# Optimization experiments

Hardware: AMD Instinct MI355X
Metric: run time of the kernel (lower is better)

## Reference

```python
import jax, jax.numpy as jnp
import numpy as np

N = 100_000   # nodes
E = 800_000   # directed edges
D = 300       # emb_dim
L = 5         # num GIN layers
G = 4096      # graphs in batch
FEAT = 512
PROJ = 256
EPS = 1e-5


def setup_inputs() -> dict:
    key = jax.random.key(0)
    ks = jax.random.split(key, 20)
    s = 0.05
    return {
        "atom_type": jax.random.randint(ks[0], (N,), 0, 119, dtype=jnp.int32),
        "chirality": jax.random.randint(ks[1], (N,), 0, 3, dtype=jnp.int32),
        "edge_index": jax.random.randint(ks[2], (2, E), 0, N, dtype=jnp.int32),
        "bond_type": jax.random.randint(ks[3], (E,), 0, 4, dtype=jnp.int32),
        "bond_dir": jax.random.randint(ks[4], (E,), 0, 3, dtype=jnp.int32),
        "batch": jnp.sort(jax.random.randint(ks[5], (N,), 0, G, dtype=jnp.int32)),
        "x_emb1": jax.random.normal(ks[6], (119, D), jnp.float32) * s,
        "x_emb2": jax.random.normal(ks[7], (3, D), jnp.float32) * s,
        "ee1": jax.random.normal(ks[8], (L, 5, D), jnp.float32) * s,
        "ee2": jax.random.normal(ks[9], (L, 3, D), jnp.float32) * s,
        "W1": jax.random.normal(ks[10], (L, D, 2 * D), jnp.float32) * s,
        "b1": jnp.zeros((L, 2 * D), jnp.float32),
        "W2": jax.random.normal(ks[11], (L, 2 * D, D), jnp.float32) * s,
        "b2": jnp.zeros((L, D), jnp.float32),
        "gamma": jnp.ones((L, D), jnp.float32),
        "beta": jnp.zeros((L, D), jnp.float32),
        "feat_W": jax.random.normal(ks[12], (D, FEAT), jnp.float32) * s,
        "feat_b": jnp.zeros((FEAT,), jnp.float32),
        "proj_W": jax.random.normal(ks[13], (FEAT, PROJ), jnp.float32) * s,
        "proj_b": jnp.zeros((PROJ,), jnp.float32),
    }


def _encoder(atom_type, chirality, edge_index, bond_type, bond_dir, batch,
             x_emb1, x_emb2, ee1, ee2, W1, b1, W2, b2, gamma, beta,
             feat_W, feat_b, proj_W, proj_b):
    # Initial node embedding: x_embedding1(x[:,0]) + x_embedding2(x[:,1])
    h = x_emb1[atom_type] + x_emb2[chirality]            # [N, D]
    row, col = edge_index[0], edge_index[1]
    for l in range(L):
        # edge embeddings for real edges
        ee = ee1[l][bond_type] + ee2[l][bond_dir]        # [E, D]
        # gather + add + scatter-sum over real edges
        msgs = h[col] + ee                               # [E, D]
        agg = jax.ops.segment_sum(msgs, row, num_segments=N)  # [N, D]
        # self-loop edges have attr [4, 0] -> constant embedding per layer
        agg = agg + h + (ee1[l, 4] + ee2[l, 0])
        # 2-layer MLP
        hid = jax.nn.relu(agg @ W1[l] + b1[l])
        h2 = hid @ W2[l] + b2[l]
        # BatchNorm1d (training mode: batch statistics, biased variance)
        mean = jnp.mean(h2, axis=0)
        var = jnp.var(h2, axis=0)
        h = gamma[l] * (h2 - mean) * jax.lax.rsqrt(var + EPS) + beta[l]
        if l < L - 1:
            h = jax.nn.relu(h)
    # global mean pool per graph
    sums = jax.ops.segment_sum(h, batch, num_segments=G)              # [G, D]
    counts = jax.ops.segment_sum(jnp.ones((N, 1), h.dtype), batch, num_segments=G)
    pooled = sums / jnp.maximum(counts, 1.0)
    feat = pooled @ feat_W + feat_b                                    # [G, FEAT]
    return feat @ proj_W + proj_b                                      # [G, PROJ]


def reference(atom_type, chirality, edge_index, bond_type, bond_dir, batch,
              x_emb1, x_emb2, ee1, ee2, W1, b1, W2, b2, gamma, beta,
              feat_W, feat_b, proj_W, proj_b):
    return _encoder(atom_type, chirality, edge_index, bond_type, bond_dir, batch,
                    x_emb1, x_emb2, ee1, ee2, W1, b1, W2, b2, gamma, beta,
                    feat_W, feat_b, proj_W, proj_b)
```

## Files before the change

kernel.cpp:

```cpp
#include <hip/hip_runtime.h>
#include <hip/hip_bf16.h>

typedef __bf16 bf16_t;
typedef bf16_t bf16x8 __attribute__((ext_vector_type(8)));
typedef float f32x4 __attribute__((ext_vector_type(4)));

#define D_DIM 300
#define HSTRIDE 304
#define CSTRIDE 304
#define ROWU 152
#define AROWU 160
#define TPB 320

__device__ inline f32x4 mfma16(bf16x8 a, bf16x8 b, f32x4 c) {
  return __builtin_amdgcn_mfma_f32_16x16x32_bf16(a, b, c, 0, 0, 0);
}

__device__ inline void split2(float x, unsigned short& h, unsigned short& l) {
  bf16_t hb = (bf16_t)x;
  float hf = (float)hb;
  bf16_t lb = (bf16_t)(x - hf);
  h = __builtin_bit_cast(unsigned short, hb);
  l = __builtin_bit_cast(unsigned short, lb);
}

__device__ inline uint4 pack8(const unsigned short* s) {
  return make_uint4((unsigned int)s[0] | ((unsigned int)s[1] << 16),
                    (unsigned int)s[2] | ((unsigned int)s[3] << 16),
                    (unsigned int)s[4] | ((unsigned int)s[5] << 16),
                    (unsigned int)s[6] | ((unsigned int)s[7] << 16));
}

__device__ inline unsigned int packbf2(float x0, float x1) {
  unsigned short a = __builtin_bit_cast(unsigned short, (bf16_t)x0);
  unsigned short b = __builtin_bit_cast(unsigned short, (bf16_t)x1);
  return (unsigned int)a | ((unsigned int)b << 16);
}

__device__ inline float bfu_lo(unsigned int u) {
  unsigned int x = u << 16;
  float f;
  __builtin_memcpy(&f, &x, 4);
  return f;
}

__device__ inline float bfu_hi(unsigned int u) {
  unsigned int x = u & 0xffff0000u;
  float f;
  __builtin_memcpy(&f, &x, 4);
  return f;
}


__global__ void zero_u32_kernel(unsigned int* __restrict__ p, long long n) {
  long long i = (long long)blockIdx.x * blockDim.x + threadIdx.x;
  long long s = (long long)gridDim.x * blockDim.x;
  for (; i < n; i += s) p[i] = 0u;
}


__global__ void init_h_kernel(const int* __restrict__ atom, const int* __restrict__ chir,
                              const float* __restrict__ e1, const float* __restrict__ e2,
                              unsigned int* __restrict__ hb) {
  int n = blockIdx.x;
  int t = threadIdx.x;
  if (t >= ROWU) return;
  int d = t * 2;
  unsigned int out = 0u;
  if (d < D_DIM) {
    int a = atom[n], c = chir[n];
    float x0 = e1[a * D_DIM + d] + e2[c * D_DIM + d];
    float x1 = e1[a * D_DIM + d + 1] + e2[c * D_DIM + d + 1];
    out = packbf2(x0, x1);
  }
  hb[(size_t)n * ROWU + t] = out;
}

__global__ void combo_kernel(const float* __restrict__ ee1, const float* __restrict__ ee2,
                             float* __restrict__ ct) {
  int l = blockIdx.x / 13, c = blockIdx.x % 13;
  int d = threadIdx.x;
  if (d >= CSTRIDE) return;
  int bt = (c < 12) ? (c / 3) : 4;
  int bd = (c < 12) ? (c % 3) : 0;
  float v = 0.f;
  if (d < D_DIM)
    v = ee1[(size_t)(l * 5 + bt) * D_DIM + d] + ee2[(size_t)(l * 3 + bd) * D_DIM + d];
  ct[((size_t)(l * 13 + c)) * CSTRIDE + d] = v;
}

__global__ void edge_combo_kernel(const int* __restrict__ bt, const int* __restrict__ bd,
                                  int* __restrict__ ec, int E) {
  int e = blockIdx.x * blockDim.x + threadIdx.x;
  if (e < E) ec[e] = bt[e] * 3 + bd[e];
}


__global__ void csr_count_kernel(const int* __restrict__ row, int* __restrict__ deg, int E) {
  int e = blockIdx.x * blockDim.x + threadIdx.x;
  if (e < E) atomicAdd(&deg[row[e]], 1);
}

#define SBLK 1024
__global__ void scan1_kernel(const int* __restrict__ deg, int* __restrict__ off,
                             int* __restrict__ btot, int n) {
  __shared__ int buf[SBLK];
  int t = threadIdx.x;
  int i = blockIdx.x * SBLK + t;
  int v = (i < n) ? deg[i] : 0;
  buf[t] = v;
  __syncthreads();
#pragma unroll
  for (int s = 1; s < SBLK; s <<= 1) {
    int add = (t >= s) ? buf[t - s] : 0;
    __syncthreads();
    buf[t] += add;
    __syncthreads();
  }
  if (i < n) off[i] = buf[t] - v;
  if (t == SBLK - 1) btot[blockIdx.x] = buf[t];
}

__global__ void scan2_kernel(int* __restrict__ btot, int* __restrict__ off, int n, int nb) {
  __shared__ int buf[128];
  int t = threadIdx.x;
  int v = (t < nb) ? btot[t] : 0;
  buf[t] = v;
  __syncthreads();
#pragma unroll
  for (int s = 1; s < 128; s <<= 1) {
    int add = (t >= s) ? buf[t - s] : 0;
    __syncthreads();
    buf[t] += add;
    __syncthreads();
  }
  if (t < nb) btot[t] = buf[t] - v;
  if (t == nb - 1) off[n] = buf[t];
}

__global__ void scan3_kernel(int* __restrict__ off, int* __restrict__ cur,
                             const int* __restrict__ btot, int n) {
  int i = blockIdx.x * SBLK + threadIdx.x;
  if (i < n) {
    int v = off[i] + btot[blockIdx.x];
    off[i] = v;
    cur[i] = v;
  }
}

__global__ void csr_fill_kernel(const int* __restrict__ row, const int* __restrict__ col,
                                const int* __restrict__ ec, int* __restrict__ cur,
                                unsigned int* __restrict__ pck, int E) {
  int e = blockIdx.x * blockDim.x + threadIdx.x;
  if (e < E) {
    int r = row[e];
    int p = atomicAdd(&cur[r], 1);
    pck[p] = ((unsigned int)col[e] << 4) | (unsigned int)ec[e];
  }
}


__global__ void goff_kernel(const int* __restrict__ batch, int* __restrict__ goff, int N, int G) {
  int n = blockIdx.x * blockDim.x + threadIdx.x;
  if (n >= N) return;
  if (n == 0) {
    int g1 = batch[0];
    for (int g = 0; g <= g1; ++g) goff[g] = 0;
  } else {
    int g0 = batch[n - 1], g1 = batch[n];
    for (int g = g0 + 1; g <= g1; ++g) goff[g] = n;
  }
  if (n == N - 1) {
    int g0 = batch[N - 1];
    for (int g = g0 + 1; g <= G; ++g) goff[g] = N;
  }
}


__global__ void affine_kernel(const float* __restrict__ h2, const float* __restrict__ sc,
                              const float* __restrict__ sh, unsigned int* __restrict__ hb,
                              long long total) {
  long long i = (long long)blockIdx.x * blockDim.x + threadIdx.x;
  long long s = (long long)gridDim.x * blockDim.x;
  for (; i < total; i += s) {
    int cu = (int)(i % ROWU);
    long long n = i / ROWU;
    int d = cu * 2;
    unsigned int out = 0u;
    if (d < D_DIM) {
      float2 v = *(const float2*)(h2 + n * HSTRIDE + d);
      float x0 = fmaxf(fmaf(v.x, sc[d], sh[d]), 0.f);
      float x1 = fmaxf(fmaf(v.y, sc[d + 1], sh[d + 1]), 0.f);
      out = packbf2(x0, x1);
    }
    hb[i] = out;
  }
}


__global__ __launch_bounds__(256) void gather_kernel(
    const unsigned int* __restrict__ hb, const int* __restrict__ off,
    const unsigned int* __restrict__ pck, const float* __restrict__ ct_l,
    unsigned int* __restrict__ agg, int N) {
  int wid = threadIdx.x >> 6;
  int lane = threadIdx.x & 63;
  int n = blockIdx.x * 4 + wid;
  if (n >= N) return;
  const bool act = lane < 38;
  const int u4 = lane * 4;

  float a0[4] = {0.f, 0.f, 0.f, 0.f};
  float a1[4] = {0.f, 0.f, 0.f, 0.f};

  if (act) {
    uint4 hv = *(const uint4*)(hb + (size_t)n * ROWU + u4);
    const float* c12 = ct_l + 12 * CSTRIDE + lane * 8;
    float4 cv0 = ((const float4*)c12)[0];
    float4 cv1 = ((const float4*)c12)[1];
    a0[0] = bfu_lo(hv.x) + cv0.x; a1[0] = bfu_hi(hv.x) + cv0.y;
    a0[1] = bfu_lo(hv.y) + cv0.z; a1[1] = bfu_hi(hv.y) + cv0.w;
    a0[2] = bfu_lo(hv.z) + cv1.x; a1[2] = bfu_hi(hv.z) + cv1.y;
    a0[3] = bfu_lo(hv.w) + cv1.z; a1[3] = bfu_hi(hv.w) + cv1.w;
  }

  int p0 = off[n], p1 = off[n + 1];
  int p = p0;
  for (; p + 2 <= p1; p += 2) {
    unsigned int k0 = pck[p];
    unsigned int k1 = pck[p + 1];
    if (act) {
      uint4 h0 = *(const uint4*)(hb + (size_t)(k0 >> 4) * ROWU + u4);
      uint4 h1 = *(const uint4*)(hb + (size_t)(k1 >> 4) * ROWU + u4);
      const float* c0 = ct_l + (k0 & 15u) * CSTRIDE + lane * 8;
      const float* c1 = ct_l + (k1 & 15u) * CSTRIDE + lane * 8;
      float4 c0a = ((const float4*)c0)[0];
      float4 c0b = ((const float4*)c0)[1];
      float4 c1a = ((const float4*)c1)[0];
      float4 c1b = ((const float4*)c1)[1];
      a0[0] += bfu_lo(h0.x) + c0a.x; a1[0] += bfu_hi(h0.x) + c0a.y;
      a0[1] += bfu_lo(h0.y) + c0a.z; a1[1] += bfu_hi(h0.y) + c0a.w;
      a0[2] += bfu_lo(h0.z) + c0b.x; a1[2] += bfu_hi(h0.z) + c0b.y;
      a0[3] += bfu_lo(h0.w) + c0b.z; a1[3] += bfu_hi(h0.w) + c0b.w;
      a0[0] += bfu_lo(h1.x) + c1a.x; a1[0] += bfu_hi(h1.x) + c1a.y;
      a0[1] += bfu_lo(h1.y) + c1a.z; a1[1] += bfu_hi(h1.y) + c1a.w;
      a0[2] += bfu_lo(h1.z) + c1b.x; a1[2] += bfu_hi(h1.z) + c1b.y;
      a0[3] += bfu_lo(h1.w) + c1b.z; a1[3] += bfu_hi(h1.w) + c1b.w;
    }
  }
  if (p < p1) {
    unsigned int k0 = pck[p];
    if (act) {
      uint4 h0 = *(const uint4*)(hb + (size_t)(k0 >> 4) * ROWU + u4);
      const float* c0 = ct_l + (k0 & 15u) * CSTRIDE + lane * 8;
      float4 c0a = ((const float4*)c0)[0];
      float4 c0b = ((const float4*)c0)[1];
      a0[0] += bfu_lo(h0.x) + c0a.x; a1[0] += bfu_hi(h0.x) + c0a.y;
      a0[1] += bfu_lo(h0.y) + c0a.z; a1[1] += bfu_hi(h0.y) + c0a.w;
      a0[2] += bfu_lo(h0.z) + c0b.x; a1[2] += bfu_hi(h0.z) + c0b.y;
      a0[3] += bfu_lo(h0.w) + c0b.z; a1[3] += bfu_hi(h0.w) + c0b.w;
    }
  }

  unsigned int* ao = agg + (size_t)n * AROWU;
  if (act) {
    uint4 o;
    o.x = packbf2(a0[0], a1[0]);
    o.y = packbf2(a0[1], a1[1]);
    o.z = packbf2(a0[2], a1[2]);
    o.w = packbf2(a0[3], a1[3]);
    *(uint4*)(ao + u4) = o;
  } else if (lane < 40) {
    *(uint4*)(ao + u4) = make_uint4(0, 0, 0, 0);
  }
}


__global__ void bn_final_kernel(const float* __restrict__ stats, const float* __restrict__ gamma_l,
                                const float* __restrict__ beta_l, float* __restrict__ bnsc,
                                float* __restrict__ bnsh, int N) {
  int d = threadIdx.x;
  if (d >= D_DIM) return;
  float inv_n = 1.0f / (float)N;
  float mean = stats[d] * inv_n;
  float var = stats[D_DIM + d] * inv_n - mean * mean;
  float inv = rsqrtf(var + 1e-5f);
  float sc = gamma_l[d] * inv;
  bnsc[d] = sc;
  bnsh[d] = beta_l[d] - mean * sc;
}


__global__ void pool_seg_kernel(const float* __restrict__ h, const float* __restrict__ sc,
                                const float* __restrict__ sh, const int* __restrict__ goff,
                                float* __restrict__ pool) {
  int g = blockIdx.x;
  int d = threadIdx.x;
  if (d >= D_DIM) return;
  int s = goff[g], e = goff[g + 1];
  float scv = sc[d], shv = sh[d];
  float acc = 0.f;
  for (int n = s; n < e; ++n) acc += fmaf(h[(size_t)n * HSTRIDE + d], scv, shv);
  float cnt = (float)(e - s);
  if (cnt < 1.f) cnt = 1.f;
  pool[(size_t)g * D_DIM + d] = acc / cnt;
}


__global__ void wpack_kernel(const float* __restrict__ W, bf16_t* __restrict__ Th,
                             bf16_t* __restrict__ Tl, int K, int Nw) {
  int ct = blockIdx.x;
  int ks = blockIdx.y;
  int l = threadIdx.x;
  int col = ct * 16 + (l & 15);
  int kb = ks * 32 + (l >> 4) * 8;
  unsigned short hs[8], ls[8];
#pragma unroll
  for (int j = 0; j < 8; ++j) {
    int k = kb + j;
    float v = (k < K && col < Nw) ? W[(size_t)k * Nw + col] : 0.f;
    split2(v, hs[j], ls[j]);
  }
  size_t off = ((size_t)(ct * gridDim.y + ks) * 64 + l) * 8;
  *(uint4*)(Th + off) = pack8(hs);
  *(uint4*)(Tl + off) = pack8(ls);
}


template <int KP, int KV, bool RELU, bool OUT_BF16, bool STATS>
__global__ __launch_bounds__(256, 4) void mfma_gemm10(
    const unsigned short* __restrict__ A, const bf16_t* __restrict__ Bh,
    const bf16_t* __restrict__ Bl, const float* __restrict__ bias, void* __restrict__ Cptr,
    float* __restrict__ stats, int M, int Nc, int astride, int cstride, int nx, int nyT) {
  constexpr int KSTEPS = KP / 32;
  constexpr int PLANE = 128 * 80;
  __shared__ __align__(16) char lds[2 * PLANE];

  int dd = blockIdx.x;
  int xcd = dd & 7;
  int q = dd >> 3;
  int xt = q % nx;
  int yt = (q / nx) * 8 + xcd;
  if (yt >= nyT) return;
  const int m0 = yt * 128;
  const int n0 = xt * 64;
  const int nb16 = n0 >> 4;

  const int t = threadIdx.x;
  const int w = t >> 6;
  const int lane = t & 63;
  const int wm = w >> 1, wn = w & 1;
  const int lrow = lane & 15;
  const int lk = lane >> 4;

  const int sr = t >> 1;
  const int skh = (t & 1) * 16;
  int gr = m0 + sr;
  if (gr >= M) gr = M - 1;
  const unsigned short* arow = A + (size_t)gr * astride + skh;
  const int soff = sr * 80 + (t & 1) * 32;

  const bf16_t* bp0h = Bh + ((size_t)(nb16 + wn * 2 + 0) * KSTEPS * 64 + lane) * 8;
  const bf16_t* bp1h = Bh + ((size_t)(nb16 + wn * 2 + 1) * KSTEPS * 64 + lane) * 8;
  const bf16_t* bp0l = Bl + ((size_t)(nb16 + wn * 2 + 0) * KSTEPS * 64 + lane) * 8;
  const bf16_t* bp1l = Bl + ((size_t)(nb16 + wn * 2 + 1) * KSTEPS * 64 + lane) * 8;

  f32x4 acc[4][2] = {};

  {
    uint4 v0 = ((const uint4*)arow)[0];
    uint4 v1 = ((const uint4*)arow)[1];
    *(uint4*)(lds + soff) = v0;
    *(uint4*)(lds + soff + 16) = v1;
  }
  bf16x8 bhc0 = *(const bf16x8*)(const void*)bp0h;
  bf16x8 bhc1 = *(const bf16x8*)(const void*)bp1h;
  bf16x8 blc0 = *(const bf16x8*)(const void*)bp0l;
  bf16x8 blc1 = *(const bf16x8*)(const void*)bp1l;
  __builtin_amdgcn_sched_barrier(0);
  asm volatile("s_waitcnt lgkmcnt(0)");
  __builtin_amdgcn_s_barrier();
  __builtin_amdgcn_sched_barrier(0);

#pragma unroll
  for (int kt = 0; kt < KSTEPS; ++kt) {
    const int cur = kt & 1;
    uint4 n0v, n1v;
    bf16x8 bhn0, bhn1, bln0, bln1;
    if (kt + 1 < KSTEPS) {
      const uint4* p = (const uint4*)(arow + (kt + 1) * 32);
      n0v = p[0];
      n1v = p[1];
      if (KV < KP) {
        int kg = (kt + 1) * 32 + skh;
        if (kg >= KV) n0v = make_uint4(0, 0, 0, 0);
        if (kg + 8 >= KV) n1v = make_uint4(0, 0, 0, 0);
      }
      int bs = (kt + 1) * 512;
      bhn0 = *(const bf16x8*)(const void*)(bp0h + bs);
      bhn1 = *(const bf16x8*)(const void*)(bp1h + bs);
      bln0 = *(const bf16x8*)(const void*)(bp0l + bs);
      bln1 = *(const bf16x8*)(const void*)(bp1l + bs);
    }
    const char* lbase = lds + cur * PLANE;
    bf16x8 ah[4];
#pragma unroll
    for (int i = 0; i < 4; ++i) {
      int row = wm * 64 + i * 16 + lrow;
      ah[i] = *(const bf16x8*)(const void*)(lbase + row * 80 + lk * 16);
    }
#pragma unroll
    for (int i = 0; i < 4; ++i) {
      acc[i][0] = mfma16(ah[i], bhc0, acc[i][0]);
      acc[i][0] = mfma16(ah[i], blc0, acc[i][0]);
      acc[i][1] = mfma16(ah[i], bhc1, acc[i][1]);
      acc[i][1] = mfma16(ah[i], blc1, acc[i][1]);
    }
    if (kt + 1 < KSTEPS) {
      char* sn = lds + (cur ^ 1) * PLANE + soff;
      *(uint4*)(sn) = n0v;
      *(uint4*)(sn + 16) = n1v;
      __builtin_amdgcn_sched_barrier(0);
      asm volatile("s_waitcnt lgkmcnt(0)");
      __builtin_amdgcn_s_barrier();
      __builtin_amdgcn_sched_barrier(0);
      bhc0 = bhn0;
      bhc1 = bhn1;
      blc0 = bln0;
      blc1 = bln1;
    }
  }

#pragma unroll
  for (int j = 0; j < 2; ++j) {
    int gcol = n0 + wn * 32 + j * 16 + lrow;
    bool colok = gcol < Nc;
    float bsv = colok ? bias[gcol] : 0.f;
    float s = 0.f, s2 = 0.f;
#pragma unroll
    for (int i = 0; i < 4; ++i) {
#pragma unroll
      for (int r4 = 0; r4 < 4; ++r4) {
        int grow = m0 + wm * 64 + i * 16 + lk * 4 + r4;
        if (grow < M && colok) {
          float v = acc[i][j][r4] + bsv;
          if (RELU) v = fmaxf(v, 0.f);
          if constexpr (STATS) {
            s += v;
            s2 += v * v;
          }
          if constexpr (OUT_BF16)
            ((bf16_t*)Cptr)[(size_t)grow * cstride + gcol] = (bf16_t)v;
          else
            ((float*)Cptr)[(size_t)grow * cstride + gcol] = v;
        }
      }
    }
    if constexpr (STATS) {
      s += __shfl_xor(s, 16);
      s += __shfl_xor(s, 32);
      s2 += __shfl_xor(s2, 16);
      s2 += __shfl_xor(s2, 32);
      if (lk == 0 && colok) {
        atomicAdd(&stats[gcol], s);
        atomicAdd(&stats[D_DIM + gcol], s2);
      }
    }
  }
}


template <int KP, bool RELU, bool OUT_BF16>
__global__ __launch_bounds__(256, 4) void mfma_gemm6(
    const char* __restrict__ A0, const bf16_t* __restrict__ Bh, const bf16_t* __restrict__ Bl,
    const float* __restrict__ bias, void* __restrict__ Cptr, int M, int Nc, int K, int abytes,
    int cstride, int nx, int nyT) {
  constexpr int KSTEPS = KP / 32;
  constexpr int PLANE = 128 * 80;
  __shared__ __align__(16) char lds[2 * PLANE];

  int dd = blockIdx.x;
  int xcd = dd & 7;
  int q = dd >> 3;
  int xt = q % nx;
  int yt = (q / nx) * 8 + xcd;
  if (yt >= nyT) return;
  const int m0 = yt * 128;
  const int n0 = xt * 64;
  const int nb16 = n0 >> 4;

  const int t = threadIdx.x;
  const int w = t >> 6;
  const int lane = t & 63;
  const int wm = w >> 1, wn = w & 1;
  const int lrow = lane & 15;
  const int lk = lane >> 4;

  const int sr = t >> 1;
  const int skh = (t & 1) * 16;
  const int gr = m0 + sr;
  char* sdst = lds + sr * 80 + (t & 1) * 32;

  f32x4 acc[4][2] = {};

  for (int kt = 0; kt < KSTEPS; ++kt) {
    const int kg = kt * 32 + skh;
    float va[16];
    if (gr < M && kg + 16 <= K) {
      const float4* fp = (const float4*)(A0 + (size_t)gr * abytes + kg * 4);
#pragma unroll
      for (int qd = 0; qd < 4; ++qd) {
        float4 x = fp[qd];
        va[4 * qd] = x.x;
        va[4 * qd + 1] = x.y;
        va[4 * qd + 2] = x.z;
        va[4 * qd + 3] = x.w;
      }
    } else {
#pragma unroll
      for (int j = 0; j < 16; ++j)
        va[j] = (gr < M && kg + j < K) ? *(const float*)(A0 + (size_t)gr * abytes + (kg + j) * 4)
                                       : 0.f;
    }
    unsigned short hs[16], ls[16];
#pragma unroll
    for (int j = 0; j < 16; ++j) split2(va[j], hs[j], ls[j]);
    *(uint4*)(sdst) = pack8(hs);
    *(uint4*)(sdst + 16) = pack8(hs + 8);
    *(uint4*)(sdst + PLANE) = pack8(ls);
    *(uint4*)(sdst + PLANE + 16) = pack8(ls + 8);
    __syncthreads();
    bf16x8 ah[4], al[4];
#pragma unroll
    for (int i = 0; i < 4; ++i) {
      int row = wm * 64 + i * 16 + lrow;
      ah[i] = *(const bf16x8*)(const void*)(lds + row * 80 + lk * 16);
      al[i] = *(const bf16x8*)(const void*)(lds + PLANE + row * 80 + lk * 16);
    }
#pragma unroll
    for (int j = 0; j < 2; ++j) {
      int ct16 = nb16 + wn * 2 + j;
      size_t bo = ((size_t)(ct16 * KSTEPS + kt) * 64 + lane) * 8;
      bf16x8 bh = *(const bf16x8*)(const void*)(Bh + bo);
      bf16x8 bl = *(const bf16x8*)(const void*)(Bl + bo);
#pragma unroll
      for (int i = 0; i < 4; ++i) {
        acc[i][j] = mfma16(ah[i], bh, acc[i][j]);
        acc[i][j] = mfma16(ah[i], bl, acc[i][j]);
        acc[i][j] = mfma16(al[i], bh, acc[i][j]);
      }
    }
    __syncthreads();
  }

#pragma unroll
  for (int j = 0; j < 2; ++j) {
    int gcol = n0 + wn * 32 + j * 16 + lrow;
    if (gcol >= Nc) continue;
    float bsv = bias[gcol];
#pragma unroll
    for (int i = 0; i < 4; ++i) {
#pragma unroll
      for (int r4 = 0; r4 < 4; ++r4) {
        int grow = m0 + wm * 64 + i * 16 + lk * 4 + r4;
        if (grow < M) {
          float v = acc[i][j][r4] + bsv;
          if (RELU) v = fmaxf(v, 0.f);
          if constexpr (OUT_BF16)
            ((bf16_t*)Cptr)[(size_t)grow * cstride + gcol] = (bf16_t)v;
          else
            ((float*)Cptr)[(size_t)grow * cstride + gcol] = v;
        }
      }
    }
  }
}


extern "C" void kernel_launch(void* const* d_in, const int* in_sizes, int n_in,
                              void* d_out, int out_size, void* d_ws, size_t ws_size,
                              hipStream_t stream) {
  const int* atom = (const int*)d_in[0];
  const int* chir = (const int*)d_in[1];
  const int* eidx = (const int*)d_in[2];
  const int* btype = (const int*)d_in[3];
  const int* bdir = (const int*)d_in[4];
  const int* batch = (const int*)d_in[5];
  const float* x_emb1 = (const float*)d_in[6];
  const float* x_emb2 = (const float*)d_in[7];
  const float* ee1 = (const float*)d_in[8];
  const float* ee2 = (const float*)d_in[9];
  const float* W1 = (const float*)d_in[10];
  const float* b1 = (const float*)d_in[11];
  const float* W2 = (const float*)d_in[12];
  const float* b2 = (const float*)d_in[13];
  const float* gamma = (const float*)d_in[14];
  const float* beta = (const float*)d_in[15];
  const float* featW = (const float*)d_in[16];
  const float* featb = (const float*)d_in[17];
  const float* projW = (const float*)d_in[18];
  const float* projb = (const float*)d_in[19];

  const int N = in_sizes[0];
  const int E = in_sizes[2] / 2;
  const int PROJ = in_sizes[19];
  const int FEAT = in_sizes[17];
  const int G = out_size / PROJ;
  const int L = in_sizes[11] / (2 * D_DIM);
  const int D2 = 2 * D_DIM;

  const int* row = eidx;
  const int* col = eidx + E;

  const int CT16_1 = 40, KS_1 = 10;
  const int CT16_2 = 20, KS_2 = 19;
  const int CT16_F = 32, KS_F = 10;
  const int CT16_P = 16, KS_P = 16;
  const int SZ1 = CT16_1 * KS_1 * 512;
  const int SZ2 = CT16_2 * KS_2 * 512;
  const int SZF = CT16_F * KS_F * 512;
  const int SZP = CT16_P * KS_P * 512;

  char* ws = (char*)d_ws;
  size_t off = 0;
  auto alloc = [&](size_t bytes) -> char* {
    char* p = ws + off;
    off += (bytes + 255) & ~(size_t)255;
    return p;
  };
  char* R1 = alloc((size_t)N * 1216);
  char* R2 = alloc((size_t)N * 1216);
  float* CT = (float*)alloc((size_t)L * 13 * CSTRIDE * 4);
  int* EC = (int*)alloc((size_t)E * 4);
  int* DEG = (int*)alloc((size_t)N * 4);
  int* OFF = (int*)alloc((size_t)(N + 1) * 4);
  int* CUR = (int*)alloc((size_t)N * 4);
  int* BTOT = (int*)alloc(512);
  unsigned int* PCK = (unsigned int*)alloc((size_t)E * 4);
  int* GOFF = (int*)alloc((size_t)(G + 1) * 4);
  float* STATS = (float*)alloc(2 * D_DIM * 4);
  float* BNSC = (float*)alloc(D_DIM * 4);
  float* BNSH = (float*)alloc(D_DIM * 4);
  bf16_t* W1Th = (bf16_t*)alloc((size_t)L * SZ1 * 2);
  bf16_t* W1Tl = (bf16_t*)alloc((size_t)L * SZ1 * 2);
  bf16_t* W2Th = (bf16_t*)alloc((size_t)L * SZ2 * 2);
  bf16_t* W2Tl = (bf16_t*)alloc((size_t)L * SZ2 * 2);
  bf16_t* FTh = (bf16_t*)alloc((size_t)SZF * 2);
  bf16_t* FTl = (bf16_t*)alloc((size_t)SZF * 2);
  bf16_t* PTh = (bf16_t*)alloc((size_t)SZP * 2);
  bf16_t* PTl = (bf16_t*)alloc((size_t)SZP * 2);
  (void)ws_size;

  unsigned int* HBF = (unsigned int*)R2;
  unsigned int* AGG = (unsigned int*)R1;
  float* H2 = (float*)R1;
  char* HID = R2;

  init_h_kernel<<<N, 256, 0, stream>>>(atom, chir, x_emb1, x_emb2, HBF);
  combo_kernel<<<L * 13, TPB, 0, stream>>>(ee1, ee2, CT);
  edge_combo_kernel<<<(E + 255) / 256, 256, 0, stream>>>(btype, bdir, EC, E);

  const int nb = (N + SBLK - 1) / SBLK;
  zero_u32_kernel<<<(N + 255) / 256, 256, 0, stream>>>((unsigned int*)DEG, N);
  csr_count_kernel<<<(E + 255) / 256, 256, 0, stream>>>(row, DEG, E);
  scan1_kernel<<<nb, SBLK, 0, stream>>>(DEG, OFF, BTOT, N);
  scan2_kernel<<<1, 128, 0, stream>>>(BTOT, OFF, N, nb);
  scan3_kernel<<<nb, SBLK, 0, stream>>>(OFF, CUR, BTOT, N);
  csr_fill_kernel<<<(E + 255) / 256, 256, 0, stream>>>(row, col, EC, CUR, PCK, E);
  goff_kernel<<<(N + 255) / 256, 256, 0, stream>>>(batch, GOFF, N, G);

  for (int l = 0; l < L; ++l) {
    wpack_kernel<<<dim3(CT16_1, KS_1), 64, 0, stream>>>(
        W1 + (size_t)l * D_DIM * D2, W1Th + (size_t)l * SZ1, W1Tl + (size_t)l * SZ1, D_DIM, D2);
    wpack_kernel<<<dim3(CT16_2, KS_2), 64, 0, stream>>>(
        W2 + (size_t)l * D2 * D_DIM, W2Th + (size_t)l * SZ2, W2Tl + (size_t)l * SZ2, D2, D_DIM);
  }
  wpack_kernel<<<dim3(CT16_F, KS_F), 64, 0, stream>>>(featW, FTh, FTl, D_DIM, FEAT);
  wpack_kernel<<<dim3(CT16_P, KS_P), 64, 0, stream>>>(projW, PTh, PTl, FEAT, PROJ);

  const int nyT = (N + 127) / 128;
  const int ny8 = ((nyT + 7) / 8) * 8;
  const int nyG = (G + 127) / 128;
  const int nyG8 = ((nyG + 7) / 8) * 8;
  const long long HTOT = (long long)N * ROWU;

  for (int l = 0; l < L; ++l) {
    const float* ctl = CT + (size_t)l * 13 * CSTRIDE;
    gather_kernel<<<(N + 3) / 4, 256, 0, stream>>>(HBF, OFF, PCK, ctl, AGG, N);
    mfma_gemm10<320, 320, true, true, false><<<10 * ny8, 256, 0, stream>>>(
        (const unsigned short*)R1, W1Th + (size_t)l * SZ1, W1Tl + (size_t)l * SZ1,
        b1 + (size_t)l * D2, HID, nullptr, N, D2, 320, 608, 10, nyT);
    zero_u32_kernel<<<2, 320, 0, stream>>>((unsigned int*)STATS, 2 * D_DIM);
    mfma_gemm10<608, 600, false, false, true><<<5 * ny8, 256, 0, stream>>>(
        (const unsigned short*)HID, W2Th + (size_t)l * SZ2, W2Tl + (size_t)l * SZ2,
        b2 + (size_t)l * D_DIM, H2, STATS, N, D_DIM, 608, HSTRIDE, 5, nyT);
    bn_final_kernel<<<1, TPB, 0, stream>>>(STATS, gamma + (size_t)l * D_DIM,
                                           beta + (size_t)l * D_DIM, BNSC, BNSH, N);
    if (l < L - 1)
      affine_kernel<<<2048, 256, 0, stream>>>(H2, BNSC, BNSH, HBF, HTOT);
  }

  float* POOL = (float*)R2;
  float* FEATB = POOL + (size_t)G * D_DIM;

  pool_seg_kernel<<<G, TPB, 0, stream>>>(H2, BNSC, BNSH, GOFF, POOL);

  mfma_gemm6<320, false, false><<<8 * nyG8, 256, 0, stream>>>(
      (const char*)POOL, FTh, FTl, featb, FEATB, G, FEAT, D_DIM, 1200, FEAT, 8, nyG);
  mfma_gemm6<512, false, false><<<4 * nyG8, 256, 0, stream>>>(
      (const char*)FEATB, PTh, PTl, projb, d_out, G, PROJ, FEAT, 2048, PROJ, 4, nyG);
}
```

Measured before the change: 2.128 ms.

## Fuse BatchNorm affine+ReLU into gather and store GEMM2 output as bf16

The second GEMM now writes its pre-BatchNorm output as bf16 into a separate buffer instead of fp32. The separate affine kernel is removed. The next layer's gather applies the BN scale/shift and ReLU to each gathered neighbour row on the fly, and pooling reads the bf16 buffer. This removes one full read/write pass over the node features per layer and halves the GEMM2 output traffic. In exchange, the affine math is recomputed once per edge rather than once per node, and the BN statistics and pooling now operate on bf16-rounded values.

Measured after the change: 2.131 ms. No clear change (+0.1%).

```diff
diff --git a/kernel.cpp b/kernel.cpp
--- a/kernel.cpp
+++ b/kernel.cpp
@@ -46,6 +46,13 @@
 
 __device__ inline float bfu_hi(unsigned int u) {
   unsigned int x = u & 0xffff0000u;
+  float f;
+  __builtin_memcpy(&f, &x, 4);
+  return f;
+}
+
+__device__ inline float bf16tof(unsigned short us) {
+  unsigned int x = (unsigned int)us << 16;
   float f;
   __builtin_memcpy(&f, &x, 4);
   return f;
@@ -177,29 +184,10 @@
 }
 
 
-__global__ void affine_kernel(const float* __restrict__ h2, const float* __restrict__ sc,
-                              const float* __restrict__ sh, unsigned int* __restrict__ hb,
-                              long long total) {
-  long long i = (long long)blockIdx.x * blockDim.x + threadIdx.x;
-  long long s = (long long)gridDim.x * blockDim.x;
-  for (; i < total; i += s) {
-    int cu = (int)(i % ROWU);
-    long long n = i / ROWU;
-    int d = cu * 2;
-    unsigned int out = 0u;
-    if (d < D_DIM) {
-      float2 v = *(const float2*)(h2 + n * HSTRIDE + d);
-      float x0 = fmaxf(fmaf(v.x, sc[d], sh[d]), 0.f);
-      float x1 = fmaxf(fmaf(v.y, sc[d + 1], sh[d + 1]), 0.f);
-      out = packbf2(x0, x1);
-    }
-    hb[i] = out;
-  }
-}
-
-
+template <bool TRANS>
 __global__ __launch_bounds__(256) void gather_kernel(
-    const unsigned int* __restrict__ hb, const int* __restrict__ off,
+    const unsigned int* __restrict__ hb, const float* __restrict__ sc,
+    const float* __restrict__ sh, const int* __restrict__ off,
     const unsigned int* __restrict__ pck, const float* __restrict__ ct_l,
     unsigned int* __restrict__ agg, int N) {
   int wid = threadIdx.x >> 6;
@@ -209,18 +197,57 @@
   const bool act = lane < 38;
   const int u4 = lane * 4;
 
+  float scv[8], shv[8];
+  if constexpr (TRANS) {
+    if (act) {
+      float4 s0 = ((const float4*)(sc + lane * 8))[0];
+      float4 s1 = ((const float4*)(sc + lane * 8))[1];
+      float4 t0 = ((const float4*)(sh + lane * 8))[0];
+      float4 t1 = ((const float4*)(sh + lane * 8))[1];
+      scv[0] = s0.x; scv[1] = s0.y; scv[2] = s0.z; scv[3] = s0.w;
+      scv[4] = s1.x; scv[5] = s1.y; scv[6] = s1.z; scv[7] = s1.w;
+      shv[0] = t0.x; shv[1] = t0.y; shv[2] = t0.z; shv[3] = t0.w;
+      shv[4] = t1.x; shv[5] = t1.y; shv[6] = t1.z; shv[7] = t1.w;
+    }
+  }
+
   float a0[4] = {0.f, 0.f, 0.f, 0.f};
   float a1[4] = {0.f, 0.f, 0.f, 0.f};
 
+#define ACCROW(HV, CP)                                                        \
+  do {                                                                        \
+    float4 ca = ((const float4*)(CP))[0];                                     \
+    float4 cb = ((const float4*)(CP))[1];                                     \
+    float xl, xh;                                                             \
+    xl = bfu_lo((HV).x); xh = bfu_hi((HV).x);                                 \
+    if constexpr (TRANS) {                                                    \
+      xl = fmaxf(fmaf(xl, scv[0], shv[0]), 0.f);                              \
+      xh = fmaxf(fmaf(xh, scv[1], shv[1]), 0.f);                              \
+    }                                                                         \
+    a0[0] += xl + ca.x; a1[0] += xh + ca.y;                                   \
+    xl = bfu_lo((HV).y); xh = bfu_hi((HV).y);                                 \
+    if constexpr (TRANS) {                                                    \
+      xl = fmaxf(fmaf(xl, scv[2], shv[2]), 0.f);                              \
+      xh = fmaxf(fmaf(xh, scv[3], shv[3]), 0.f);                              \
+    }                                                                         \
+    a0[1] += xl + ca.z; a1[1] += xh + ca.w;                                   \
+    xl = bfu_lo((HV).z); xh = bfu_hi((HV).z);                                 \
+    if constexpr (TRANS) {                                                    \
+      xl = fmaxf(fmaf(xl, scv[4], shv[4]), 0.f);                              \
+      xh = fmaxf(fmaf(xh, scv[5], shv[5]), 0.f);                              \
+    }                                                                         \
+    a0[2] += xl + cb.x; a1[2] += xh + cb.y;                                   \
+    xl = bfu_lo((HV).w); xh = bfu_hi((HV).w);                                 \
+    if constexpr (TRANS) {                                                    \
+      xl = fmaxf(fmaf(xl, scv[6], shv[6]), 0.f);                              \
+      xh = fmaxf(fmaf(xh, scv[7], shv[7]), 0.f);                              \
+    }                                                                         \
+    a0[3] += xl + cb.z; a1[3] += xh + cb.w;                                   \
+  } while (0)
+
   if (act) {
     uint4 hv = *(const uint4*)(hb + (size_t)n * ROWU + u4);
-    const float* c12 = ct_l + 12 * CSTRIDE + lane * 8;
-    float4 cv0 = ((const float4*)c12)[0];
-    float4 cv1 = ((const float4*)c12)[1];
-    a0[0] = bfu_lo(hv.x) + cv0.x; a1[0] = bfu_hi(hv.x) + cv0.y;
-    a0[1] = bfu_lo(hv.y) + cv0.z; a1[1] = bfu_hi(hv.y) + cv0.w;
-    a0[2] = bfu_lo(hv.z) + cv1.x; a1[2] = bfu_hi(hv.z) + cv1.y;
-    a0[3] = bfu_lo(hv.w) + cv1.z; a1[3] = bfu_hi(hv.w) + cv1.w;
+    ACCROW(hv, ct_l + 12 * CSTRIDE + lane * 8);
   }
 
   int p0 = off[n], p1 = off[n + 1];
@@ -231,35 +258,18 @@
     if (act) {
       uint4 h0 = *(const uint4*)(hb + (size_t)(k0 >> 4) * ROWU + u4);
       uint4 h1 = *(const uint4*)(hb + (size_t)(k1 >> 4) * ROWU + u4);
-      const float* c0 = ct_l + (k0 & 15u) * CSTRIDE + lane * 8;
-      const float* c1 = ct_l + (k1 & 15u) * CSTRIDE + lane * 8;
-      float4 c0a = ((const float4*)c0)[0];
-      float4 c0b = ((const float4*)c0)[1];
-      float4 c1a = ((const float4*)c1)[0];
-      float4 c1b = ((const float4*)c1)[1];
-      a0[0] += bfu_lo(h0.x) + c0a.x; a1[0] += bfu_hi(h0.x) + c0a.y;
-      a0[1] += bfu_lo(h0.y) + c0a.z; a1[1] += bfu_hi(h0.y) + c0a.w;
-      a0[2] += bfu_lo(h0.z) + c0b.x; a1[2] += bfu_hi(h0.z) + c0b.y;
-      a0[3] += bfu_lo(h0.w) + c0b.z; a1[3] += bfu_hi(h0.w) + c0b.w;
-      a0[0] += bfu_lo(h1.x) + c1a.x; a1[0] += bfu_hi(h1.x) + c1a.y;
-      a0[1] += bfu_lo(h1.y) + c1a.z; a1[1] += bfu_hi(h1.y) + c1a.w;
-      a0[2] += bfu_lo(h1.z) + c1b.x; a1[2] += bfu_hi(h1.z) + c1b.y;
-      a0[3] += bfu_lo(h1.w) + c1b.z; a1[3] += bfu_hi(h1.w) + c1b.w;
+      ACCROW(h0, ct_l + (k0 & 15u) * CSTRIDE + lane * 8);
+      ACCROW(h1, ct_l + (k1 & 15u) * CSTRIDE + lane * 8);
     }
   }
   if (p < p1) {
     unsigned int k0 = pck[p];
     if (act) {
       uint4 h0 = *(const uint4*)(hb + (size_t)(k0 >> 4) * ROWU + u4);
-      const float* c0 = ct_l + (k0 & 15u) * CSTRIDE + lane * 8;
-      float4 c0a = ((const float4*)c0)[0];
-      float4 c0b = ((const float4*)c0)[1];
-      a0[0] += bfu_lo(h0.x) + c0a.x; a1[0] += bfu_hi(h0.x) + c0a.y;
-      a0[1] += bfu_lo(h0.y) + c0a.z; a1[1] += bfu_hi(h0.y) + c0a.w;
-      a0[2] += bfu_lo(h0.z) + c0b.x; a1[2] += bfu_hi(h0.z) + c0b.y;
-      a0[3] += bfu_lo(h0.w) + c0b.z; a1[3] += bfu_hi(h0.w) + c0b.w;
-    }
-  }
+      ACCROW(h0, ct_l + (k0 & 15u) * CSTRIDE + lane * 8);
+    }
+  }
+#undef ACCROW
 
   unsigned int* ao = agg + (size_t)n * AROWU;
   if (act) {
@@ -290,16 +300,16 @@
 }
 
 
-__global__ void pool_seg_kernel(const float* __restrict__ h, const float* __restrict__ sc,
-                                const float* __restrict__ sh, const int* __restrict__ goff,
-                                float* __restrict__ pool) {
+__global__ void pool_seg_kernel(const unsigned short* __restrict__ h2b,
+                                const float* __restrict__ sc, const float* __restrict__ sh,
+                                const int* __restrict__ goff, float* __restrict__ pool) {
   int g = blockIdx.x;
   int d = threadIdx.x;
   if (d >= D_DIM) return;
   int s = goff[g], e = goff[g + 1];
   float scv = sc[d], shv = sh[d];
   float acc = 0.f;
-  for (int n = s; n < e; ++n) acc += fmaf(h[(size_t)n * HSTRIDE + d], scv, shv);
+  for (int n = s; n < e; ++n) acc += fmaf(bf16tof(h2b[(size_t)n * HSTRIDE + d]), scv, shv);
   float cnt = (float)(e - s);
   if (cnt < 1.f) cnt = 1.f;
   pool[(size_t)g * D_DIM + d] = acc / cnt;
@@ -627,8 +637,9 @@
     off += (bytes + 255) & ~(size_t)255;
     return p;
   };
-  char* R1 = alloc((size_t)N * 1216);
+  char* R1 = alloc((size_t)N * 640);
   char* R2 = alloc((size_t)N * 1216);
+  char* R3 = alloc((size_t)N * 608);
   float* CT = (float*)alloc((size_t)L * 13 * CSTRIDE * 4);
   int* EC = (int*)alloc((size_t)E * 4);
   int* DEG = (int*)alloc((size_t)N * 4);
@@ -650,12 +661,11 @@
   bf16_t* PTl = (bf16_t*)alloc((size_t)SZP * 2);
   (void)ws_size;
 
-  unsigned int* HBF = (unsigned int*)R2;
   unsigned int* AGG = (unsigned int*)R1;
-  float* H2 = (float*)R1;
   char* HID = R2;
-
-  init_h_kernel<<<N, 256, 0, stream>>>(atom, chir, x_emb1, x_emb2, HBF);
+  unsigned int* H2B = (unsigned int*)R3;
+
+  init_h_kernel<<<N, 256, 0, stream>>>(atom, chir, x_emb1, x_emb2, H2B);
   combo_kernel<<<L * 13, TPB, 0, stream>>>(ee1, ee2, CT);
   edge_combo_kernel<<<(E + 255) / 256, 256, 0, stream>>>(btype, bdir, EC, E);
 
@@ -681,28 +691,30 @@
   const int ny8 = ((nyT + 7) / 8) * 8;
   const int nyG = (G + 127) / 128;
   const int nyG8 = ((nyG + 7) / 8) * 8;
-  const long long HTOT = (long long)N * ROWU;
 
   for (int l = 0; l < L; ++l) {
     const float* ctl = CT + (size_t)l * 13 * CSTRIDE;
-    gather_kernel<<<(N + 3) / 4, 256, 0, stream>>>(HBF, OFF, PCK, ctl, AGG, N);
+    if (l == 0)
+      gather_kernel<false><<<(N + 3) / 4, 256, 0, stream>>>(H2B, BNSC, BNSH, OFF, PCK, ctl,
+                                                            AGG, N);
+    else
+      gather_kernel<true><<<(N + 3) / 4, 256, 0, stream>>>(H2B, BNSC, BNSH, OFF, PCK, ctl,
+                                                           AGG, N);
     mfma_gemm10<320, 320, true, true, false><<<10 * ny8, 256, 0, stream>>>(
         (const unsigned short*)R1, W1Th + (size_t)l * SZ1, W1Tl + (size_t)l * SZ1,
         b1 + (size_t)l * D2, HID, nullptr, N, D2, 320, 608, 10, nyT);
     zero_u32_kernel<<<2, 320, 0, stream>>>((unsigned int*)STATS, 2 * D_DIM);
-    mfma_gemm10<608, 600, false, false, true><<<5 * ny8, 256, 0, stream>>>(
+    mfma_gemm10<608, 600, false, true, true><<<5 * ny8, 256, 0, stream>>>(
         (const unsigned short*)HID, W2Th + (size_t)l * SZ2, W2Tl + (size_t)l * SZ2,
-        b2 + (size_t)l * D_DIM, H2, STATS, N, D_DIM, 608, HSTRIDE, 5, nyT);
+        b2 + (size_t)l * D_DIM, H2B, STATS, N, D_DIM, 608, HSTRIDE, 5, nyT);
     bn_final_kernel<<<1, TPB, 0, stream>>>(STATS, gamma + (size_t)l * D_DIM,
                                            beta + (size_t)l * D_DIM, BNSC, BNSH, N);
-    if (l < L - 1)
-      affine_kernel<<<2048, 256, 0, stream>>>(H2, BNSC, BNSH, HBF, HTOT);
   }
 
   float* POOL = (float*)R2;
   float* FEATB = POOL + (size_t)G * D_DIM;
 
-  pool_seg_kernel<<<G, TPB, 0, stream>>>(H2, BNSC, BNSH, GOFF, POOL);
+  pool_seg_kernel<<<G, TPB, 0, stream>>>((const unsigned short*)H2B, BNSC, BNSH, GOFF, POOL);
 
   mfma_gemm6<320, false, false><<<8 * nyG8, 256, 0, stream>>>(
       (const char*)POOL, FTh, FTl, featb, FEATB, G, FEAT, D_DIM, 1200, FEAT, 8, nyG);
```
